# Kernel tuning notes

Hardware: AMD Instinct MI355X
Metric: run time of the kernel (lower is better)

Reference implementation:

```python
import jax, jax.numpy as jnp
import numpy as np

EPS = 1e-5
CHUNK = 512


def _bn(x, gamma, beta):
    # BatchNorm1d in training mode: biased batch statistics over the batch dim
    m = x.mean(axis=0)
    v = ((x - m) ** 2).mean(axis=0)
    return (x - m) * jax.lax.rsqrt(v + EPS) * gamma + beta


def _xavier(k, fan_in, fan_out):
    lim = float(np.sqrt(6.0 / (fan_in + fan_out)))
    return jax.random.uniform(k, (fan_in, fan_out), minval=-lim, maxval=lim, dtype=jnp.float32)


def setup_inputs() -> dict:
    key = jax.random.key(0)
    ks = jax.random.split(key, 10)
    B, CH_S, CH_H, T = 8192, 512, 2048, 3
    D = CH_H * T  # 6144 = 12 chunks of 512
    inp = {
        "fs": jax.random.normal(ks[0], (B, CH_S), dtype=jnp.float32),
        "ft0": jax.random.normal(ks[1], (B, CH_H), dtype=jnp.float32),
        "ft1": jax.random.normal(ks[2], (B, CH_H), dtype=jnp.float32),
        "ft2": jax.random.normal(ks[3], (B, CH_H), dtype=jnp.float32),
        # fixed (non-trainable in the original: plain tensor) score key [512, 1]
        "score_key": jax.random.uniform(ks[4], (CHUNK, 1), dtype=jnp.float32),
        # align_t: Linear(D,2048) -> BN -> Linear(2048,2048) -> BN -> Linear(2048,CH_H) -> ReLU
        "W1": _xavier(ks[5], D, 2048), "b1": jnp.zeros((2048,), jnp.float32),
        "g1": jnp.ones((2048,), jnp.float32), "beta1": jnp.zeros((2048,), jnp.float32),
        "W2": _xavier(ks[6], 2048, 2048), "b2": jnp.zeros((2048,), jnp.float32),
        "g2": jnp.ones((2048,), jnp.float32), "beta2": jnp.zeros((2048,), jnp.float32),
        "W3": _xavier(ks[7], 2048, CH_H), "b3": jnp.zeros((CH_H,), jnp.float32),
        # extend: Linear(CH_H, D) -> ReLU
        "We": _xavier(ks[8], CH_H, D), "bE": jnp.zeros((D,), jnp.float32),
    }
    return inp


def reference(fs, ft0, ft1, ft2, score_key, W1, b1, g1, beta1, W2, b2, g2, beta2, W3, b3, We, bE):
    # fs is accepted but unused, mirroring the original forward
    ft_all = jnp.concatenate([ft0, ft1, ft2], axis=1)  # [B, D]
    B, D = ft_all.shape
    n_chunks = D // CHUNK
    chunks = ft_all.reshape(B, n_chunks, CHUNK)  # [B, C, 512]
    # chunked score matmul against key[512,1], softmax over chunks
    score = jax.nn.softmax(jnp.einsum("bck,k->bc", chunks, score_key[:, 0]), axis=1)  # [B, C]
    # per-chunk reweighting: x <- x + x*score  == x*(1+score), one broadcasted multiply
    ft_all = (chunks * (1.0 + score[:, :, None])).reshape(B, D)
    # align_t MLP (BatchNorm in training mode, no activation between first layers)
    h = _bn(ft_all @ W1 + b1, g1, beta1)
    h = _bn(h @ W2 + b2, g2, beta2)
    aligned_t = jax.nn.relu(h @ W3 + b3)
    extend_t = jax.nn.relu(aligned_t @ We + bE)
    return aligned_t, extend_t, ft_all
```

## Files before the change

kernel.cpp:

```cpp
#include <hip/hip_runtime.h>
#include <hip/hip_bf16.h>
#include <cstdint>
#include <cstddef>

using bf16x8 = __attribute__((ext_vector_type(8))) __bf16;
using f32x4  = __attribute__((ext_vector_type(4))) float;

__device__ __forceinline__ unsigned short f2bf(float f) {
  unsigned int u = __float_as_uint(f);
  u += 0x7FFFu + ((u >> 16) & 1u);
  return (unsigned short)(u >> 16);
}

__device__ __forceinline__ void async_cp16(const void* g, void* l) {
  __builtin_amdgcn_global_load_lds(
      (const __attribute__((address_space(1))) unsigned int*)g,
      (__attribute__((address_space(3))) unsigned int*)l, 16, 0, 0);
}

__global__ __launch_bounds__(256) void wconv(const float* __restrict__ W,
                                             unsigned short* __restrict__ Wt,
                                             int K, int N) {
  __shared__ float tile[32][33];
  const int n0 = blockIdx.x * 32;
  const int k0 = blockIdx.y * 32;
  const int tx = threadIdx.x;
  const int ty = threadIdx.y;
  for (int i = 0; i < 32; i += 8)
    tile[ty + i][tx] = W[(size_t)(k0 + ty + i) * N + n0 + tx];
  __syncthreads();
  for (int i = 0; i < 32; i += 8)
    Wt[(size_t)(n0 + ty + i) * K + k0 + tx] = f2bf(tile[tx][ty + i]);
}

__global__ __launch_bounds__(256) void score_kernel(
    const float* __restrict__ ft0, const float* __restrict__ ft1,
    const float* __restrict__ ft2, const float* __restrict__ key,
    float* __restrict__ out_f, unsigned short* __restrict__ out_b) {
  const int row  = blockIdx.x;
  const int t    = threadIdx.x;
  const int lane = t & 63;
  const int w    = t >> 6;
  const int h    = t >> 7;
  __shared__ float wsum[6][4];
  __shared__ float mult[12];

  const float4* k4 = (const float4*)key;
  float4 v[6];
#pragma unroll
  for (int i = 0; i < 6; i++) {
    const int idx4 = t + 256 * i;
    const int e    = idx4 * 4;
    const float* tsrc = (i < 2) ? ft0 : (i < 4) ? ft1 : ft2;
    v[i] = *(const float4*)(tsrc + (size_t)row * 2048 + (e & 2047));
    float4 kv = k4[idx4 & 127];
    float p = v[i].x * kv.x + v[i].y * kv.y + v[i].z * kv.z + v[i].w * kv.w;
#pragma unroll
    for (int o = 32; o > 0; o >>= 1) p += __shfl_down(p, o, 64);
    if (lane == 0) wsum[i][w] = p;
  }
  __syncthreads();
  if (t == 0) {
    float s[12];
    float mx = -1e30f;
    for (int c = 0; c < 12; c++) {
      s[c] = wsum[c >> 1][2 * (c & 1)] + wsum[c >> 1][2 * (c & 1) + 1];
      mx = fmaxf(mx, s[c]);
    }
    float tot = 0.f;
    for (int c = 0; c < 12; c++) { s[c] = expf(s[c] - mx); tot += s[c]; }
    const float inv = 1.0f / tot;
    for (int c = 0; c < 12; c++) mult[c] = 1.0f + s[c] * inv;
  }
  __syncthreads();
#pragma unroll
  for (int i = 0; i < 6; i++) {
    const int idx4 = t + 256 * i;
    const int e    = idx4 * 4;
    const float m  = mult[2 * i + h];
    float4 o;
    o.x = v[i].x * m; o.y = v[i].y * m; o.z = v[i].z * m; o.w = v[i].w * m;
    *(float4*)(out_f + (size_t)row * 6144 + e) = o;
    ushort4 ob;
    ob.x = f2bf(o.x); ob.y = f2bf(o.y); ob.z = f2bf(o.z); ob.w = f2bf(o.w);
    *(ushort4*)(out_b + (size_t)row * 6144 + e) = ob;
  }
}

template <int EPI>
__global__ __launch_bounds__(512, 2) void gemm256(
    const unsigned short* __restrict__ A,
    const unsigned short* __restrict__ Bt,
    const float* __restrict__ bias,
    float* __restrict__ C,
    unsigned short* __restrict__ Cbf,
    int M, int N, int K) {
  __shared__ __align__(16) unsigned short smem[65536];
  const int t    = threadIdx.x;
  const int lane = t & 63;
  const int w    = t >> 6;
  const int wm   = w >> 2;
  const int wn   = w & 3;
  const int frow = lane & 15;
  const int quad = lane >> 4;
  const size_t m0 = (size_t)blockIdx.y * 256;
  const size_t n0 = (size_t)blockIdx.x * 256;

  const bool isB  = w >= 4;
  const int  seg  = (w & 3) * 4096;
  const int  off0 = seg + lane * 16;
  const int  pos0 = off0 ^ (((off0 >> 7) & 7) << 4);
  const int  r0   = pos0 >> 6;
  const int  kb0  = pos0 & 63;
  const unsigned short* gp =
      (isB ? Bt + (n0 + (size_t)r0) * K : A + (m0 + (size_t)r0) * K) + (kb0 >> 1);
  char* lseg = (char*)smem + (isB ? 16384 : 0) + seg;

  const int offA = (wm * 128 + frow) * 64 + quad * 16;
  const int aoff = offA ^ (((offA >> 7) & 7) << 4);
  const int offB = (wn * 64 + frow) * 64 + quad * 16;
  const int boff = 16384 + (offB ^ (((offB >> 7) & 7) << 4));

  f32x4 acc[8][4];
  const f32x4 z = {0.f, 0.f, 0.f, 0.f};
#pragma unroll
  for (int i = 0; i < 8; i++)
#pragma unroll
    for (int j = 0; j < 4; j++) acc[i][j] = z;

  const int nkt = K >> 5;

  auto stage = [&](int slot) {
    char* lb = lseg + slot * 32768;
    async_cp16(gp,                  lb);
    async_cp16(gp + (size_t)16 * K, lb + 1024);
    async_cp16(gp + (size_t)32 * K, lb + 2048);
    async_cp16(gp + (size_t)48 * K, lb + 3072);
    gp += 32;
  };

  auto compute = [&](int slot) {
    const char* base = (const char*)smem + slot * 32768;
    bf16x8 af[8], bv[4];
#pragma unroll
    for (int mi = 0; mi < 8; ++mi)
      af[mi] = *(const bf16x8*)(base + aoff + mi * 1024);
#pragma unroll
    for (int ni = 0; ni < 4; ++ni)
      bv[ni] = *(const bf16x8*)(base + boff + ni * 1024);
    __builtin_amdgcn_s_setprio(1);
#pragma unroll
    for (int mi = 0; mi < 8; ++mi)
#pragma unroll
      for (int ni = 0; ni < 4; ++ni)
        acc[mi][ni] = __builtin_amdgcn_mfma_f32_16x16x32_bf16(af[mi], bv[ni], acc[mi][ni], 0, 0, 0);
    __builtin_amdgcn_s_setprio(0);
  };

  stage(0); stage(1); stage(2);
  int kt = 0;
  for (; kt + 3 < nkt; ++kt) {
    stage((kt + 3) & 3);
    asm volatile("s_waitcnt vmcnt(12)" ::: "memory");
    asm volatile("s_barrier" ::: "memory");
    compute(kt & 3);
    asm volatile("s_waitcnt lgkmcnt(0)\n\ts_barrier" ::: "memory");
  }
  asm volatile("s_waitcnt vmcnt(8)" ::: "memory");
  asm volatile("s_barrier" ::: "memory");
  compute(kt & 3); ++kt;
  asm volatile("s_waitcnt vmcnt(4)" ::: "memory");
  asm volatile("s_barrier" ::: "memory");
  compute(kt & 3); ++kt;
  asm volatile("s_waitcnt vmcnt(0)" ::: "memory");
  asm volatile("s_barrier" ::: "memory");
  compute(kt & 3);

#pragma unroll
  for (int mi = 0; mi < 8; ++mi) {
    const size_t rowb = m0 + wm * 128 + mi * 16 + quad * 4;
#pragma unroll
    for (int ni = 0; ni < 4; ++ni) {
      const size_t col = n0 + wn * 64 + ni * 16 + frow;
      const float bvs = bias[col];
#pragma unroll
      for (int r = 0; r < 4; ++r) {
        float v = acc[mi][ni][r] + bvs;
        if (EPI == 1) v = fmaxf(v, 0.f);
        const size_t idx = (rowb + r) * (size_t)N + col;
        C[idx] = v;
        if (EPI == 1 && Cbf != nullptr) Cbf[idx] = f2bf(v);
      }
    }
  }
}

__global__ __launch_bounds__(256) void bn_accum(const float* __restrict__ h,
                                                float* __restrict__ ps,
                                                float* __restrict__ pq, int N) {
  const int c  = blockIdx.x * 256 + threadIdx.x;
  const int r0 = blockIdx.y * 256;
  const float* p = h + (size_t)r0 * N + c;
  float s = 0.f, q = 0.f;
  for (int r = 0; r < 256; r++) {
    float x = p[(size_t)r * N];
    s += x; q += x * x;
  }
  ps[(size_t)blockIdx.y * N + c] = s;
  pq[(size_t)blockIdx.y * N + c] = q;
}

__global__ __launch_bounds__(256) void bn_final(const float* __restrict__ ps,
                                                const float* __restrict__ pq,
                                                const float* __restrict__ g,
                                                const float* __restrict__ beta,
                                                float* __restrict__ stats,
                                                int N, int nb, float invM) {
  const int c = blockIdx.x * 256 + threadIdx.x;
  float s = 0.f, q = 0.f;
  for (int b = 0; b < nb; b++) { s += ps[(size_t)b * N + c]; q += pq[(size_t)b * N + c]; }
  const float mean = s * invM;
  const float var  = q * invM - mean * mean;
  const float sc   = g[c] * rsqrtf(var + 1e-5f);
  stats[c]     = sc;
  stats[N + c] = beta[c] - mean * sc;
}

__global__ __launch_bounds__(256) void bn_norm(const float* __restrict__ h,
                                               const float* __restrict__ stats,
                                               unsigned short* __restrict__ hb, int N) {
  const size_t i4 = (size_t)blockIdx.x * 256 + threadIdx.x;
  const float4 x = ((const float4*)h)[i4];
  const int c = (int)((i4 * 4) & (size_t)(N - 1));
  const float4 sc = *(const float4*)(stats + c);
  const float4 tt = *(const float4*)(stats + N + c);
  ushort4 ob;
  ob.x = f2bf(x.x * sc.x + tt.x);
  ob.y = f2bf(x.y * sc.y + tt.y);
  ob.z = f2bf(x.z * sc.z + tt.z);
  ob.w = f2bf(x.w * sc.w + tt.w);
  ((ushort4*)hb)[i4] = ob;
}

extern "C" void kernel_launch(void* const* d_in, const int* in_sizes, int n_in,
                              void* d_out, int out_size, void* d_ws, size_t ws_size,
                              hipStream_t stream) {
  const float* ft0 = (const float*)d_in[1];
  const float* ft1 = (const float*)d_in[2];
  const float* ft2 = (const float*)d_in[3];
  const float* key = (const float*)d_in[4];
  const float* W1  = (const float*)d_in[5];
  const float* b1  = (const float*)d_in[6];
  const float* g1  = (const float*)d_in[7];
  const float* be1 = (const float*)d_in[8];
  const float* W2  = (const float*)d_in[9];
  const float* b2  = (const float*)d_in[10];
  const float* g2  = (const float*)d_in[11];
  const float* be2 = (const float*)d_in[12];
  const float* W3  = (const float*)d_in[13];
  const float* b3  = (const float*)d_in[14];
  const float* We  = (const float*)d_in[15];
  const float* bE  = (const float*)d_in[16];

  float* out         = (float*)d_out;
  float* out_aligned = out;
  float* out_extend  = out + (size_t)8192 * 2048;
  float* out_ft      = out + (size_t)8192 * 2048 + (size_t)8192 * 6144;

  char* ws = (char*)d_ws;
  unsigned short* ft_bf = (unsigned short*)(ws);
  unsigned short* Wt1   = (unsigned short*)(ws + 100663296ull);
  unsigned short* Wt2   = (unsigned short*)(ws + 125829120ull);
  unsigned short* Wt3   = (unsigned short*)(ws + 134217728ull);
  unsigned short* WtE   = (unsigned short*)(ws + 142606336ull);
  float*          hf    = (float*)(ws + 167772160ull);
  unsigned short* hba   = (unsigned short*)(ws + 234881024ull);
  unsigned short* hbb   = (unsigned short*)(ws + 268435456ull);
  float*          psum  = (float*)(ws + 301989888ull);
  float*          psq   = (float*)(ws + 302252032ull);
  float*          stats = (float*)(ws + 302514176ull);

  const dim3 blk32(32, 8);
  wconv<<<dim3(2048 / 32, 6144 / 32), blk32, 0, stream>>>(W1, Wt1, 6144, 2048);
  wconv<<<dim3(2048 / 32, 2048 / 32), blk32, 0, stream>>>(W2, Wt2, 2048, 2048);
  wconv<<<dim3(2048 / 32, 2048 / 32), blk32, 0, stream>>>(W3, Wt3, 2048, 2048);
  wconv<<<dim3(6144 / 32, 2048 / 32), blk32, 0, stream>>>(We, WtE, 2048, 6144);

  score_kernel<<<dim3(8192), dim3(256), 0, stream>>>(ft0, ft1, ft2, key, out_ft, ft_bf);

  gemm256<0><<<dim3(8, 32), dim3(512), 0, stream>>>(ft_bf, Wt1, b1, hf,
                                                    (unsigned short*)nullptr, 8192, 2048, 6144);
  bn_accum<<<dim3(8, 32), dim3(256), 0, stream>>>(hf, psum, psq, 2048);
  bn_final<<<dim3(8), dim3(256), 0, stream>>>(psum, psq, g1, be1, stats, 2048, 32, 1.0f / 8192.0f);
  bn_norm<<<dim3(16384), dim3(256), 0, stream>>>(hf, stats, hba, 2048);

  gemm256<0><<<dim3(8, 32), dim3(512), 0, stream>>>(hba, Wt2, b2, hf,
                                                    (unsigned short*)nullptr, 8192, 2048, 2048);
  bn_accum<<<dim3(8, 32), dim3(256), 0, stream>>>(hf, psum, psq, 2048);
  bn_final<<<dim3(8), dim3(256), 0, stream>>>(psum, psq, g2, be2, stats, 2048, 32, 1.0f / 8192.0f);
  bn_norm<<<dim3(16384), dim3(256), 0, stream>>>(hf, stats, hba, 2048);

  gemm256<1><<<dim3(8, 32), dim3(512), 0, stream>>>(hba, Wt3, b3, out_aligned, hbb,
                                                    8192, 2048, 2048);
  gemm256<1><<<dim3(24, 32), dim3(512), 0, stream>>>(hbb, WtE, bE, out_extend,
                                                     (unsigned short*)nullptr, 8192, 6144, 2048);
}
```

Before: 1.384 ms.

## Double-buffer LDS fragments in registers to overlap ds_reads with MFMA

Splits the GEMM inner step into fragment load and MFMA phases, and keeps two register fragment sets so the LDS reads for the next k-tile are issued while MFMAs for the current tile run. The main loop is unrolled by two, with one barrier per k-step instead of two, and a reworked prologue and epilogue. This is meant to hide LDS latency and cut barrier stalls. The cost is doubled fragment registers, which may lower occupancy or cause spills, and the loop assumes an even tile-count parity with more complex slot indexing.

Result: faster. 1.333 ms (-3.7%).

```diff
diff --git a/kernel.cpp b/kernel.cpp
--- a/kernel.cpp
+++ b/kernel.cpp
@@ -139,42 +139,53 @@
     gp += 32;
   };
 
-  auto compute = [&](int slot) {
+  auto ldfrag = [&](int slot, bf16x8* fa, bf16x8* fb) {
     const char* base = (const char*)smem + slot * 32768;
-    bf16x8 af[8], bv[4];
 #pragma unroll
     for (int mi = 0; mi < 8; ++mi)
-      af[mi] = *(const bf16x8*)(base + aoff + mi * 1024);
+      fa[mi] = *(const bf16x8*)(base + aoff + mi * 1024);
 #pragma unroll
     for (int ni = 0; ni < 4; ++ni)
-      bv[ni] = *(const bf16x8*)(base + boff + ni * 1024);
+      fb[ni] = *(const bf16x8*)(base + boff + ni * 1024);
+  };
+
+  auto domfma = [&](const bf16x8* fa, const bf16x8* fb) {
     __builtin_amdgcn_s_setprio(1);
 #pragma unroll
     for (int mi = 0; mi < 8; ++mi)
 #pragma unroll
       for (int ni = 0; ni < 4; ++ni)
-        acc[mi][ni] = __builtin_amdgcn_mfma_f32_16x16x32_bf16(af[mi], bv[ni], acc[mi][ni], 0, 0, 0);
+        acc[mi][ni] = __builtin_amdgcn_mfma_f32_16x16x32_bf16(fa[mi], fb[ni], acc[mi][ni], 0, 0, 0);
     __builtin_amdgcn_s_setprio(0);
   };
 
+  bf16x8 fa0[8], fb0[4], fa1[8], fb1[4];
+
   stage(0); stage(1); stage(2);
+  asm volatile("s_waitcnt vmcnt(4)\n\ts_barrier" ::: "memory");
+  ldfrag(0, fa0, fb0);
+
   int kt = 0;
-  for (; kt + 3 < nkt; ++kt) {
+  for (; kt + 4 < nkt; kt += 2) {
     stage((kt + 3) & 3);
-    asm volatile("s_waitcnt vmcnt(12)" ::: "memory");
-    asm volatile("s_barrier" ::: "memory");
-    compute(kt & 3);
-    asm volatile("s_waitcnt lgkmcnt(0)\n\ts_barrier" ::: "memory");
-  }
-  asm volatile("s_waitcnt vmcnt(8)" ::: "memory");
-  asm volatile("s_barrier" ::: "memory");
-  compute(kt & 3); ++kt;
-  asm volatile("s_waitcnt vmcnt(4)" ::: "memory");
-  asm volatile("s_barrier" ::: "memory");
-  compute(kt & 3); ++kt;
-  asm volatile("s_waitcnt vmcnt(0)" ::: "memory");
-  asm volatile("s_barrier" ::: "memory");
-  compute(kt & 3);
+    domfma(fa0, fb0);
+    ldfrag((kt + 1) & 3, fa1, fb1);
+    asm volatile("s_waitcnt vmcnt(4)\n\ts_barrier" ::: "memory");
+    stage((kt + 4) & 3);
+    domfma(fa1, fb1);
+    ldfrag((kt + 2) & 3, fa0, fb0);
+    asm volatile("s_waitcnt vmcnt(4)\n\ts_barrier" ::: "memory");
+  }
+  stage((nkt - 1) & 3);
+  domfma(fa0, fb0);
+  ldfrag((nkt - 3) & 3, fa1, fb1);
+  asm volatile("s_waitcnt vmcnt(4)\n\ts_barrier" ::: "memory");
+  domfma(fa1, fb1);
+  ldfrag((nkt - 2) & 3, fa0, fb0);
+  asm volatile("s_waitcnt vmcnt(0)\n\ts_barrier" ::: "memory");
+  domfma(fa0, fb0);
+  ldfrag((nkt - 1) & 3, fa1, fb1);
+  domfma(fa1, fb1);
 
 #pragma unroll
   for (int mi = 0; mi < 8; ++mi) {
```
